# Optimization experiments

Measured on AMD Instinct MI355X. Metric: run time of the kernel, lower is better.

The kernel has to match this reference:

```python
import jax, jax.numpy as jnp
import numpy as np
from jax import lax

COUNT_NORM_FACTOR = 0.1


def setup_inputs() -> dict:
    key = jax.random.key(0)
    ks = jax.random.split(key, 8)
    B, NA, NT, D = 4096, 16, 16, 128
    task_embeds = jax.random.normal(ks[0], (B, NT, D), dtype=jnp.float32)
    task_nonag_counts = jax.random.uniform(ks[1], (B, NT), dtype=jnp.float32)
    agent_embeds = jax.random.normal(ks[2], (B, NA, D), dtype=jnp.float32)
    task_mask = jnp.zeros((B, NT), dtype=bool)
    agent_mask = jnp.zeros((B, NA), dtype=jnp.float32)  # 0 = active agent
    u = jax.random.uniform(ks[3], (NA, B, NT), dtype=jnp.float32,
                           minval=1e-6, maxval=1.0 - 1e-6)
    gumbels = -jnp.log(-jnp.log(u))
    W_count = jax.random.normal(ks[4], (2, D), dtype=jnp.float32) / np.sqrt(2.0)
    b_count = jnp.zeros((D,), dtype=jnp.float32)
    W_upd = jax.random.normal(ks[5], (2 * D, D), dtype=jnp.float32) / np.sqrt(2.0 * D)
    b_upd = jnp.zeros((D,), dtype=jnp.float32)
    return dict(task_embeds=task_embeds, task_nonag_counts=task_nonag_counts,
                agent_embeds=agent_embeds, task_mask=task_mask,
                agent_mask=agent_mask, gumbels=gumbels,
                W_count=W_count, b_count=b_count, W_upd=W_upd, b_upd=b_upd)


def _autoreg(task_embeds, task_nonag_counts, agent_embeds, task_mask,
             agent_mask, gumbels, W_count, b_count, W_upd, b_upd):
    B, NT, D = task_embeds.shape
    scale = jnp.sqrt(jnp.asarray(D, task_embeds.dtype))
    neg_min = jnp.finfo(task_embeds.dtype).min

    def step(carry, xs):
        te, counts = carry  # te: [B,NT,D], counts: [B,NT]
        ag_emb, g, amask = xs  # [B,D], [B,NT], [B]
        # count embedding: Linear(2, D) on stack([nonag, ag], -1)
        cnt_in = jnp.stack([task_nonag_counts, counts], axis=-1)  # [B,NT,2]
        cnt_e = cnt_in @ W_count + b_count  # [B,NT,D]
        # pointer logits
        logits = jnp.einsum('bd,btd->bt', ag_emb, te + cnt_e) / scale
        masked = jnp.where(task_mask, neg_min, logits)
        # RelaxedOneHotCategorical(temp=1).rsample via gumbel-softmax
        soft = jax.nn.softmax(masked + g, axis=-1)
        onehot = jax.nn.one_hot(jnp.argmax(soft, axis=-1), NT, dtype=soft.dtype)
        hard = onehot - lax.stop_gradient(soft) + soft
        agm = (1.0 - amask)[:, None]  # [B,1]
        hard = hard * agm
        hstop = lax.stop_gradient(hard)
        counts = counts + hstop * COUNT_NORM_FACTOR
        # embedding update: Linear(2D, D) on relu(concat([te, agent_embed]))
        upd_in = jnp.concatenate(
            [te, jnp.broadcast_to(ag_emb[:, None, :], (B, NT, D))], axis=-1)
        upd = jax.nn.relu(upd_in) @ W_upd + b_upd  # [B,NT,D]
        te = te + upd * hstop[..., None] * agm[..., None]
        return (te, counts), hard

    init = (task_embeds, jnp.zeros((B, NT), task_embeds.dtype))
    xs = (jnp.swapaxes(agent_embeds, 0, 1), gumbels, jnp.swapaxes(agent_mask, 0, 1))
    _, allocs = lax.scan(step, init, xs)  # [NA,B,NT]
    return jnp.swapaxes(allocs, 0, 1)  # [B,NA,NT]


def reference(task_embeds, task_nonag_counts, agent_embeds, task_mask,
              agent_mask, gumbels, W_count, b_count, W_upd, b_upd):
    return _autoreg(task_embeds, task_nonag_counts, agent_embeds, task_mask,
                    agent_mask, gumbels, W_count, b_count, W_upd, b_upd)
```

## Files before the change

kernel.cpp:

```cpp
#include <hip/hip_runtime.h>
#include <float.h>
#include <math.h>

#define NBATCH   4096
#define NAGENT   16
#define NTASK    16
#define DDIM     128
#define G        8
#define NTHREADS 512
#define SSEG     20

typedef float f32x2 __attribute__((ext_vector_type(2)));

template<int CTRL>
__device__ __forceinline__ float dppf(float x) {
    return __int_as_float(__builtin_amdgcn_update_dpp(
        0, __float_as_int(x), CTRL, 0xF, 0xF, true));
}
template<int CTRL>
__device__ __forceinline__ int dppi(int x) {
    return __builtin_amdgcn_update_dpp(0, x, CTRL, 0xF, 0xF, true);
}

template<int SEL>
__device__ __forceinline__ void pk_fma_b(f32x2& acc, f32x2 a, f32x2 b) {
    if constexpr (SEL == 0)
        asm("v_pk_fma_f32 %0, %1, %2, %0 op_sel:[0,0,0] op_sel_hi:[0,1,1]"
            : "+v"(acc) : "v"(a), "v"(b));
    else
        asm("v_pk_fma_f32 %0, %1, %2, %0 op_sel:[1,0,0] op_sel_hi:[1,1,1]"
            : "+v"(acc) : "v"(a), "v"(b));
}

__global__ __launch_bounds__(NTHREADS, 2)
void alloc_policy_kernel(const float* __restrict__ task_embeds,
                         const float* __restrict__ task_nonag,
                         const float* __restrict__ agent_embeds,
                         const unsigned char* __restrict__ task_mask,
                         const float* __restrict__ agent_mask,
                         const float* __restrict__ gumbels,
                         const float* __restrict__ W_count,
                         const float* __restrict__ b_count,
                         const float* __restrict__ W_upd,
                         const float* __restrict__ b_upd,
                         float* __restrict__ out)
{
    __shared__ __align__(16) float te[G][NTASK][DDIM];
    __shared__ __align__(16) float scr[G][16 * SSEG];
    __shared__ __align__(16) float4 sdots4[G][NAGENT];
    __shared__ __align__(16) float4 upd4[G];

    const int tid  = threadIdx.x;
    const int lane = tid & 63;
    const int w    = tid >> 6;
    const int b0   = blockIdx.x * G;
    const int gb_w = b0 + w;

    const bool h0 = (lane & 1) != 0;
    const bool h1 = (lane & 2) != 0;
    const bool h2 = (lane & 4) != 0;
    const bool h3 = (lane & 8) != 0;

    const int cg   = tid >> 4;
    const int iseg = tid & 15;
    const float bu = b_upd[cg * 4 + (tid & 3)];

    const float scalef = sqrtf(128.0f);

    f32x2 W01[16], W23[16];
    #pragma unroll
    for (int c = 0; c < 4; ++c)
        #pragma unroll
        for (int di = 0; di < 4; ++di) {
            const float4 wv = *(const float4*)(W_upd +
                (size_t)(iseg * 16 + c * 4 + di) * DDIM + cg * 4);
            W01[c * 4 + di] = f32x2{wv.x, wv.y};
            W23[c * 4 + di] = f32x2{wv.z, wv.w};
        }

    {
        const float4* src = (const float4*)(task_embeds + (size_t)b0 * NTASK * DDIM);
        float4* dst = (float4*)(&te[0][0][0]);
        #pragma unroll
        for (int k = 0; k < (G * NTASK * DDIM / 4) / NTHREADS; ++k)
            dst[k * NTHREADS + tid] = src[k * NTHREADS + tid];
    }

    {
        const int p = tid >> 2, q = tid & 3;
        const int g = p >> 4,  a = p & 15;
        const float* agp = agent_embeds + ((size_t)(b0 + g) * NAGENT + a) * DDIM + q * 32;
        float a0 = 0.f, a1 = 0.f, a2 = 0.f;
        #pragma unroll
        for (int c = 0; c < 8; ++c) {
            const float4 av = *(const float4*)(agp + c * 4);
            const float4 w0 = *(const float4*)(W_count + q * 32 + c * 4);
            const float4 w1 = *(const float4*)(W_count + DDIM + q * 32 + c * 4);
            const float4 bc = *(const float4*)(b_count + q * 32 + c * 4);
            a0 = fmaf(av.x, w0.x, a0); a0 = fmaf(av.y, w0.y, a0);
            a0 = fmaf(av.z, w0.z, a0); a0 = fmaf(av.w, w0.w, a0);
            a1 = fmaf(av.x, w1.x, a1); a1 = fmaf(av.y, w1.y, a1);
            a1 = fmaf(av.z, w1.z, a1); a1 = fmaf(av.w, w1.w, a1);
            a2 = fmaf(av.x, bc.x, a2); a2 = fmaf(av.y, bc.y, a2);
            a2 = fmaf(av.z, bc.z, a2); a2 = fmaf(av.w, bc.w, a2);
        }
        a0 += __shfl_xor(a0, 1); a0 += __shfl_xor(a0, 2);
        a1 += __shfl_xor(a1, 1); a1 += __shfl_xor(a1, 2);
        a2 += __shfl_xor(a2, 1); a2 += __shfl_xor(a2, 2);
        if (q == 0) sdots4[g][a] = make_float4(a0, a1, a2, 0.f);
    }

    const int tau = lane & 15;
    const float nn_my = task_nonag[gb_w * NTASK + tau];
    const unsigned char mask_my = task_mask[gb_w * NTASK + tau];
    float cc_my = 0.0f;

    const float* agbase = agent_embeds + (size_t)gb_w * NAGENT * DDIM;
    float2 ag2 = *(const float2*)(agbase + lane * 2);
    float  gum = gumbels[(size_t)gb_w * NTASK + tau];
    float  amk = agent_mask[(size_t)gb_w * NAGENT + 0];

    auto wave_dots = [&](float2 agv) -> float {
        float v[16];
        #pragma unroll
        for (int t = 0; t < 16; ++t) {
            const float2 t2 = *(const float2*)(&te[w][t][lane * 2]);
            v[t] = fmaf(agv.y, t2.y, agv.x * t2.x);
        }
        float p8[8];
        #pragma unroll
        for (int m2 = 0; m2 < 8; ++m2) {
            const float lo = v[2 * m2], hi = v[2 * m2 + 1];
            const float send = h0 ? lo : hi;
            const float mine = h0 ? hi : lo;
            p8[m2] = mine + dppf<0xB1>(send);
        }
        float p4[4];
        #pragma unroll
        for (int m2 = 0; m2 < 4; ++m2) {
            const float lo = p8[2 * m2], hi = p8[2 * m2 + 1];
            const float send = h1 ? lo : hi;
            const float mine = h1 ? hi : lo;
            p4[m2] = mine + dppf<0x4E>(send);
        }
        float p2v[2];
        #pragma unroll
        for (int m2 = 0; m2 < 2; ++m2) {
            const float lo = p4[2 * m2], hi = p4[2 * m2 + 1];
            const float send = h2 ? lo : hi;
            const float mine = h2 ? hi : lo;
            p2v[m2] = mine + __shfl_xor(send, 4);
        }
        float p1;
        {
            const float lo = p2v[0], hi = p2v[1];
            const float send = h3 ? lo : hi;
            const float mine = h3 ? hi : lo;
            p1 = mine + __shfl_xor(send, 8);
        }
        p1 += __shfl_xor(p1, 16);
        p1 += __shfl_xor(p1, 32);
        return p1;
    };

    __syncthreads();

    float p1_cur = wave_dots(ag2);

    for (int a = 0; a < NAGENT; ++a) {
        const float4 sd = sdots4[w][a];
        const float dot_total = p1_cur + fmaf(nn_my, sd.x, fmaf(cc_my, sd.y, sd.z));
        float z = dot_total / scalef;
        if (mask_my) z = -FLT_MAX;
        z = z + gum;

        float mz = z;
        mz = fmaxf(mz, dppf<0xB1>(mz));
        mz = fmaxf(mz, dppf<0x4E>(mz));
        mz = fmaxf(mz, __shfl_xor(mz, 4));
        mz = fmaxf(mz, __shfl_xor(mz, 8));
        const float e = expf(z - mz);
        float ss = e;
        ss += dppf<0xB1>(ss);
        ss += dppf<0x4E>(ss);
        ss += __shfl_xor(ss, 4);
        ss += __shfl_xor(ss, 8);
        const float sft = e / ss;

        float mx = sft;
        mx = fmaxf(mx, dppf<0xB1>(mx));
        mx = fmaxf(mx, dppf<0x4E>(mx));
        mx = fmaxf(mx, __shfl_xor(mx, 4));
        mx = fmaxf(mx, __shfl_xor(mx, 8));
        int cand = (sft == mx) ? tau : NTASK;
        cand = min(cand, dppi<0xB1>(cand));
        cand = min(cand, dppi<0x4E>(cand));
        cand = min(cand, __shfl_xor(cand, 4));
        cand = min(cand, __shfl_xor(cand, 8));
        const int bi = cand;

        const float agm = 1.0f - amk;
        const float onehot = (tau == bi) ? 1.0f : 0.0f;
        const float hh = ((onehot - sft) + sft) * agm;

        if (lane < 16)
            out[((size_t)gb_w * NAGENT + a) * NTASK + tau] = hh;
        cc_my = cc_my + hh * 0.1f;
        if (lane < 16 && tau == bi)
            upd4[w] = make_float4(__int_as_float(bi), hh, agm, 0.f);

        {
            const float2 tsel = *(const float2*)(&te[w][bi][lane * 2]);
            float2 r0, r1;
            r0.x = fmaxf(tsel.x, 0.f); r0.y = fmaxf(tsel.y, 0.f);
            r1.x = fmaxf(ag2.x, 0.f);  r1.y = fmaxf(ag2.y, 0.f);
            const int i0 = 2 * lane;
            const int i1 = 128 + 2 * lane;
            *(float2*)(&scr[w][(i0 >> 4) * SSEG + (i0 & 15)]) = r0;
            *(float2*)(&scr[w][(i1 >> 4) * SSEG + (i1 & 15)]) = r1;
        }

        const int an = (a + 1) & 15;
        const float2 ag2n = *(const float2*)(agbase + (size_t)an * DDIM + lane * 2);
        const float  gumn = gumbels[((size_t)an * NBATCH + gb_w) * NTASK + tau];
        const float  amkn = agent_mask[(size_t)gb_w * NAGENT + an];

        __syncthreads();

        f32x2 acc01[G], acc23[G];
        #pragma unroll
        for (int g = 0; g < G; ++g) { acc01[g] = f32x2{0.f, 0.f}; acc23[g] = f32x2{0.f, 0.f}; }
        #pragma unroll
        for (int c = 0; c < 4; ++c) {
            const int sb = iseg * SSEG + c * 4;
            #pragma unroll
            for (int g = 0; g < 8; ++g) {
                const float4 in4 = *(const float4*)(&scr[g][sb]);
                const f32x2 ixy = f32x2{in4.x, in4.y};
                const f32x2 izw = f32x2{in4.z, in4.w};
                pk_fma_b<0>(acc01[g], ixy, W01[c * 4 + 0]);
                pk_fma_b<1>(acc01[g], ixy, W01[c * 4 + 1]);
                pk_fma_b<0>(acc01[g], izw, W01[c * 4 + 2]);
                pk_fma_b<1>(acc01[g], izw, W01[c * 4 + 3]);
                pk_fma_b<0>(acc23[g], ixy, W23[c * 4 + 0]);
                pk_fma_b<1>(acc23[g], ixy, W23[c * 4 + 1]);
                pk_fma_b<0>(acc23[g], izw, W23[c * 4 + 2]);
                pk_fma_b<1>(acc23[g], izw, W23[c * 4 + 3]);
            }
        }
        float q16[16];
        #pragma unroll
        for (int m2 = 0; m2 < 16; ++m2) {
            const float lo = (m2 & 1) ? acc23[m2 >> 1].x : acc01[m2 >> 1].x;
            const float hi = (m2 & 1) ? acc23[m2 >> 1].y : acc01[m2 >> 1].y;
            const float send = h0 ? lo : hi;
            const float mine = h0 ? hi : lo;
            q16[m2] = mine + dppf<0xB1>(send);
        }
        float q8[8];
        #pragma unroll
        for (int m2 = 0; m2 < 8; ++m2) {
            const float lo = q16[2 * m2], hi = q16[2 * m2 + 1];
            const float send = h1 ? lo : hi;
            const float mine = h1 ? hi : lo;
            q8[m2] = mine + dppf<0x4E>(send);
        }
        float q4[4];
        #pragma unroll
        for (int m2 = 0; m2 < 4; ++m2) {
            const float lo = q8[2 * m2], hi = q8[2 * m2 + 1];
            const float send = h2 ? lo : hi;
            const float mine = h2 ? hi : lo;
            q4[m2] = mine + __shfl_xor(send, 4);
        }
        float q2[2];
        #pragma unroll
        for (int m2 = 0; m2 < 2; ++m2) {
            const float lo = q4[2 * m2], hi = q4[2 * m2 + 1];
            const float send = h3 ? lo : hi;
            const float mine = h3 ? hi : lo;
            q2[m2] = mine + __shfl_xor(send, 8);
        }

        float p1n = 0.f;
        if (a < NAGENT - 1) p1n = wave_dots(make_float2(ag2n.x, ag2n.y));

        #pragma unroll
        for (int hgi = 0; hgi < 2; ++hgi) {
            const int g = ((lane & 15) >> 2) + hgi * 4;
            const float4 u4 = upd4[g];
            const int ts = __float_as_int(u4.x);
            const float u = q2[hgi] + bu;
            const float addv = (u * u4.y) * u4.z;
            te[g][ts][cg * 4 + (tid & 3)] += addv;
        }
        __syncthreads();

        if (a < NAGENT - 1) {
            const float2 tn = *(const float2*)(&te[w][bi][lane * 2]);
            float pr = fmaf(ag2n.y, tn.y, ag2n.x * tn.x);
            pr += dppf<0xB1>(pr);
            pr += dppf<0x4E>(pr);
            pr += __shfl_xor(pr, 4);
            pr += __shfl_xor(pr, 8);
            pr += __shfl_xor(pr, 16);
            pr += __shfl_xor(pr, 32);
            p1_cur = (tau == bi) ? pr : p1n;
        }

        ag2 = ag2n; gum = gumn; amk = amkn;
    }
}

extern "C" void kernel_launch(void* const* d_in, const int* in_sizes, int n_in,
                              void* d_out, int out_size, void* d_ws, size_t ws_size,
                              hipStream_t stream) {
    const float*         task_embeds  = (const float*)d_in[0];
    const float*         task_nonag   = (const float*)d_in[1];
    const float*         agent_embeds = (const float*)d_in[2];
    const unsigned char* task_mask    = (const unsigned char*)d_in[3];
    const float*         agent_mask   = (const float*)d_in[4];
    const float*         gumbels      = (const float*)d_in[5];
    const float*         W_count      = (const float*)d_in[6];
    const float*         b_count      = (const float*)d_in[7];
    const float*         W_upd        = (const float*)d_in[8];
    const float*         b_upd        = (const float*)d_in[9];
    float* out = (float*)d_out;

    dim3 grid(NBATCH / G);
    dim3 block(NTHREADS);
    hipLaunchKernelGGL(alloc_policy_kernel, grid, block, 0, stream,
                       task_embeds, task_nonag, agent_embeds, task_mask,
                       agent_mask, gumbels, W_count, b_count, W_upd, b_upd, out);
}
```

Before: 131.2 us.

## Keep task embeddings in registers and stream W_upd from global per step

```diff
diff --git a/kernel.cpp b/kernel.cpp
--- a/kernel.cpp
+++ b/kernel.cpp
@@ -45,9 +45,9 @@
                          const float* __restrict__ b_upd,
                          float* __restrict__ out)
 {
-    __shared__ __align__(16) float te[G][NTASK][DDIM];
     __shared__ __align__(16) float scr[G][16 * SSEG];
     __shared__ __align__(16) float4 sdots4[G][NAGENT];
+    __shared__ __align__(16) float  uroute[G][DDIM];
     __shared__ __align__(16) float4 upd4[G];
 
     const int tid  = threadIdx.x;
@@ -66,24 +66,14 @@
     const float bu = b_upd[cg * 4 + (tid & 3)];
 
     const float scalef = sqrtf(128.0f);
-
-    f32x2 W01[16], W23[16];
-    #pragma unroll
-    for (int c = 0; c < 4; ++c)
-        #pragma unroll
-        for (int di = 0; di < 4; ++di) {
-            const float4 wv = *(const float4*)(W_upd +
-                (size_t)(iseg * 16 + c * 4 + di) * DDIM + cg * 4);
-            W01[c * 4 + di] = f32x2{wv.x, wv.y};
-            W23[c * 4 + di] = f32x2{wv.z, wv.w};
-        }
-
+    const float* wbase = W_upd + (size_t)(iseg * 16) * DDIM + cg * 4;
+
+    float2 te_reg[16];
     {
-        const float4* src = (const float4*)(task_embeds + (size_t)b0 * NTASK * DDIM);
-        float4* dst = (float4*)(&te[0][0][0]);
-        #pragma unroll
-        for (int k = 0; k < (G * NTASK * DDIM / 4) / NTHREADS; ++k)
-            dst[k * NTHREADS + tid] = src[k * NTHREADS + tid];
+        const float2* tb = (const float2*)(task_embeds + (size_t)gb_w * NTASK * DDIM);
+        #pragma unroll
+        for (int t = 0; t < 16; ++t)
+            te_reg[t] = tb[t * 64 + lane];
     }
 
     {
@@ -120,13 +110,13 @@
     float  gum = gumbels[(size_t)gb_w * NTASK + tau];
     float  amk = agent_mask[(size_t)gb_w * NAGENT + 0];
 
-    auto wave_dots = [&](float2 agv) -> float {
+    __syncthreads();
+
+    for (int a = 0; a < NAGENT; ++a) {
         float v[16];
         #pragma unroll
-        for (int t = 0; t < 16; ++t) {
-            const float2 t2 = *(const float2*)(&te[w][t][lane * 2]);
-            v[t] = fmaf(agv.y, t2.y, agv.x * t2.x);
-        }
+        for (int t = 0; t < 16; ++t)
+            v[t] = fmaf(ag2.y, te_reg[t].y, ag2.x * te_reg[t].x);
         float p8[8];
         #pragma unroll
         for (int m2 = 0; m2 < 8; ++m2) {
@@ -160,16 +150,9 @@
         }
         p1 += __shfl_xor(p1, 16);
         p1 += __shfl_xor(p1, 32);
-        return p1;
-    };
-
-    __syncthreads();
-
-    float p1_cur = wave_dots(ag2);
-
-    for (int a = 0; a < NAGENT; ++a) {
+
         const float4 sd = sdots4[w][a];
-        const float dot_total = p1_cur + fmaf(nn_my, sd.x, fmaf(cc_my, sd.y, sd.z));
+        const float dot_total = p1 + fmaf(nn_my, sd.x, fmaf(cc_my, sd.y, sd.z));
         float z = dot_total / scalef;
         if (mask_my) z = -FLT_MAX;
         z = z + gum;
@@ -198,6 +181,7 @@
         cand = min(cand, __shfl_xor(cand, 4));
         cand = min(cand, __shfl_xor(cand, 8));
         const int bi = cand;
+        const int bi_u = __builtin_amdgcn_readfirstlane(bi);
 
         const float agm = 1.0f - amk;
         const float onehot = (tau == bi) ? 1.0f : 0.0f;
@@ -210,7 +194,10 @@
             upd4[w] = make_float4(__int_as_float(bi), hh, agm, 0.f);
 
         {
-            const float2 tsel = *(const float2*)(&te[w][bi][lane * 2]);
+            float2 tsel = te_reg[0];
+            #pragma unroll
+            for (int t = 1; t < 16; ++t)
+                if (bi_u == t) tsel = te_reg[t];
             float2 r0, r1;
             r0.x = fmaxf(tsel.x, 0.f); r0.y = fmaxf(tsel.y, 0.f);
             r1.x = fmaxf(ag2.x, 0.f);  r1.y = fmaxf(ag2.y, 0.f);
@@ -225,6 +212,11 @@
         const float  gumn = gumbels[((size_t)an * NBATCH + gb_w) * NTASK + tau];
         const float  amkn = agent_mask[(size_t)gb_w * NAGENT + an];
 
+        float4 wA0 = *(const float4*)(wbase + 0 * DDIM);
+        float4 wA1 = *(const float4*)(wbase + 1 * DDIM);
+        float4 wA2 = *(const float4*)(wbase + 2 * DDIM);
+        float4 wA3 = *(const float4*)(wbase + 3 * DDIM);
+
         __syncthreads();
 
         f32x2 acc01[G], acc23[G];
@@ -232,21 +224,34 @@
         for (int g = 0; g < G; ++g) { acc01[g] = f32x2{0.f, 0.f}; acc23[g] = f32x2{0.f, 0.f}; }
         #pragma unroll
         for (int c = 0; c < 4; ++c) {
+            float4 wB0, wB1, wB2, wB3;
+            if (c < 3) {
+                const float* wn = wbase + (size_t)(c + 1) * 4 * DDIM;
+                wB0 = *(const float4*)(wn + 0 * DDIM);
+                wB1 = *(const float4*)(wn + 1 * DDIM);
+                wB2 = *(const float4*)(wn + 2 * DDIM);
+                wB3 = *(const float4*)(wn + 3 * DDIM);
+            }
             const int sb = iseg * SSEG + c * 4;
+            const f32x2 w01_0 = f32x2{wA0.x, wA0.y}, w23_0 = f32x2{wA0.z, wA0.w};
+            const f32x2 w01_1 = f32x2{wA1.x, wA1.y}, w23_1 = f32x2{wA1.z, wA1.w};
+            const f32x2 w01_2 = f32x2{wA2.x, wA2.y}, w23_2 = f32x2{wA2.z, wA2.w};
+            const f32x2 w01_3 = f32x2{wA3.x, wA3.y}, w23_3 = f32x2{wA3.z, wA3.w};
             #pragma unroll
             for (int g = 0; g < 8; ++g) {
                 const float4 in4 = *(const float4*)(&scr[g][sb]);
                 const f32x2 ixy = f32x2{in4.x, in4.y};
                 const f32x2 izw = f32x2{in4.z, in4.w};
-                pk_fma_b<0>(acc01[g], ixy, W01[c * 4 + 0]);
-                pk_fma_b<1>(acc01[g], ixy, W01[c * 4 + 1]);
-                pk_fma_b<0>(acc01[g], izw, W01[c * 4 + 2]);
-                pk_fma_b<1>(acc01[g], izw, W01[c * 4 + 3]);
-                pk_fma_b<0>(acc23[g], ixy, W23[c * 4 + 0]);
-                pk_fma_b<1>(acc23[g], ixy, W23[c * 4 + 1]);
-                pk_fma_b<0>(acc23[g], izw, W23[c * 4 + 2]);
-                pk_fma_b<1>(acc23[g], izw, W23[c * 4 + 3]);
+                pk_fma_b<0>(acc01[g], ixy, w01_0);
+                pk_fma_b<1>(acc01[g], ixy, w01_1);
+                pk_fma_b<0>(acc01[g], izw, w01_2);
+                pk_fma_b<1>(acc01[g], izw, w01_3);
+                pk_fma_b<0>(acc23[g], ixy, w23_0);
+                pk_fma_b<1>(acc23[g], ixy, w23_1);
+                pk_fma_b<0>(acc23[g], izw, w23_2);
+                pk_fma_b<1>(acc23[g], izw, w23_3);
             }
+            if (c < 3) { wA0 = wB0; wA1 = wB1; wA2 = wB2; wA3 = wB3; }
         }
         float q16[16];
         #pragma unroll
@@ -281,31 +286,20 @@
             const float mine = h3 ? hi : lo;
             q2[m2] = mine + __shfl_xor(send, 8);
         }
-
-        float p1n = 0.f;
-        if (a < NAGENT - 1) p1n = wave_dots(make_float2(ag2n.x, ag2n.y));
-
         #pragma unroll
         for (int hgi = 0; hgi < 2; ++hgi) {
             const int g = ((lane & 15) >> 2) + hgi * 4;
             const float4 u4 = upd4[g];
-            const int ts = __float_as_int(u4.x);
             const float u = q2[hgi] + bu;
-            const float addv = (u * u4.y) * u4.z;
-            te[g][ts][cg * 4 + (tid & 3)] += addv;
+            uroute[g][cg * 4 + (tid & 3)] = (u * u4.y) * u4.z;
         }
         __syncthreads();
 
-        if (a < NAGENT - 1) {
-            const float2 tn = *(const float2*)(&te[w][bi][lane * 2]);
-            float pr = fmaf(ag2n.y, tn.y, ag2n.x * tn.x);
-            pr += dppf<0xB1>(pr);
-            pr += dppf<0x4E>(pr);
-            pr += __shfl_xor(pr, 4);
-            pr += __shfl_xor(pr, 8);
-            pr += __shfl_xor(pr, 16);
-            pr += __shfl_xor(pr, 32);
-            p1_cur = (tau == bi) ? pr : p1n;
+        {
+            const float2 rt = *(const float2*)(&uroute[w][2 * lane]);
+            #pragma unroll
+            for (int t = 0; t < 16; ++t)
+                if (bi_u == t) { te_reg[t].x += rt.x; te_reg[t].y += rt.y; }
         }
 
         ag2 = ag2n; gum = gumn; amk = amkn;
```

Result: slower. 159.6 us (+21.7%).

## Halve block size, stream W_upd per step instead of holding it in registers

Applied to the files above, without the earlier changes.

```diff
diff --git a/kernel.cpp b/kernel.cpp
--- a/kernel.cpp
+++ b/kernel.cpp
@@ -6,8 +6,8 @@
 #define NAGENT   16
 #define NTASK    16
 #define DDIM     128
-#define G        8
-#define NTHREADS 512
+#define G        4
+#define NTHREADS 256
 #define SSEG     20
 
 typedef float f32x2 __attribute__((ext_vector_type(2)));
@@ -32,7 +32,20 @@
             : "+v"(acc) : "v"(a), "v"(b));
 }
 
-__global__ __launch_bounds__(NTHREADS, 2)
+__global__ void wperm_kernel(const float* __restrict__ W_upd,
+                             float4* __restrict__ wp) {
+    const int q    = blockIdx.x * 256 + threadIdx.x;
+    const int t    = q & 255;
+    const int rh   = q >> 8;
+    const int half = rh & 1;
+    const int row4 = rh >> 1;
+    const int i    = (t & 15) * 16 + row4;
+    const int col  = (t >> 4) * 8 + half * 4;
+    wp[q] = *(const float4*)(W_upd + (size_t)i * DDIM + col);
+}
+
+template<bool PERM>
+__global__ __launch_bounds__(NTHREADS, 4)
 void alloc_policy_kernel(const float* __restrict__ task_embeds,
                          const float* __restrict__ task_nonag,
                          const float* __restrict__ agent_embeds,
@@ -43,6 +56,7 @@
                          const float* __restrict__ b_count,
                          const float* __restrict__ W_upd,
                          const float* __restrict__ b_upd,
+                         const float4* __restrict__ wperm,
                          float* __restrict__ out)
 {
     __shared__ __align__(16) float te[G][NTASK][DDIM];
@@ -63,20 +77,9 @@
 
     const int cg   = tid >> 4;
     const int iseg = tid & 15;
-    const float bu = b_upd[cg * 4 + (tid & 3)];
+    const float bu = b_upd[cg * 8 + (lane & 7)];
 
     const float scalef = sqrtf(128.0f);
-
-    f32x2 W01[16], W23[16];
-    #pragma unroll
-    for (int c = 0; c < 4; ++c)
-        #pragma unroll
-        for (int di = 0; di < 4; ++di) {
-            const float4 wv = *(const float4*)(W_upd +
-                (size_t)(iseg * 16 + c * 4 + di) * DDIM + cg * 4);
-            W01[c * 4 + di] = f32x2{wv.x, wv.y};
-            W23[c * 4 + di] = f32x2{wv.z, wv.w};
-        }
 
     {
         const float4* src = (const float4*)(task_embeds + (size_t)b0 * NTASK * DDIM);
@@ -120,12 +123,14 @@
     float  gum = gumbels[(size_t)gb_w * NTASK + tau];
     float  amk = agent_mask[(size_t)gb_w * NAGENT + 0];
 
-    auto wave_dots = [&](float2 agv) -> float {
+    __syncthreads();
+
+    for (int a = 0; a < NAGENT; ++a) {
         float v[16];
         #pragma unroll
         for (int t = 0; t < 16; ++t) {
             const float2 t2 = *(const float2*)(&te[w][t][lane * 2]);
-            v[t] = fmaf(agv.y, t2.y, agv.x * t2.x);
+            v[t] = fmaf(ag2.y, t2.y, ag2.x * t2.x);
         }
         float p8[8];
         #pragma unroll
@@ -160,16 +165,9 @@
         }
         p1 += __shfl_xor(p1, 16);
         p1 += __shfl_xor(p1, 32);
-        return p1;
-    };
-
-    __syncthreads();
-
-    float p1_cur = wave_dots(ag2);
-
-    for (int a = 0; a < NAGENT; ++a) {
+
         const float4 sd = sdots4[w][a];
-        const float dot_total = p1_cur + fmaf(nn_my, sd.x, fmaf(cc_my, sd.y, sd.z));
+        const float dot_total = p1 + fmaf(nn_my, sd.x, fmaf(cc_my, sd.y, sd.z));
         float z = dot_total / scalef;
         if (mask_my) z = -FLT_MAX;
         z = z + gum;
@@ -227,32 +225,53 @@
 
         __syncthreads();
 
-        f32x2 acc01[G], acc23[G];
-        #pragma unroll
-        for (int g = 0; g < G; ++g) { acc01[g] = f32x2{0.f, 0.f}; acc23[g] = f32x2{0.f, 0.f}; }
+        f32x2 acc2[16];
+        #pragma unroll
+        for (int j = 0; j < 16; ++j) acc2[j] = f32x2{0.f, 0.f};
         #pragma unroll
         for (int c = 0; c < 4; ++c) {
-            const int sb = iseg * SSEG + c * 4;
+            float4 Wc[8];
+            if (PERM) {
+                const float4* wp = wperm + tid;
+                #pragma unroll
+                for (int rh = 0; rh < 8; ++rh)
+                    Wc[rh] = wp[(size_t)(c * 8 + rh) * 256];
+            } else {
+                #pragma unroll
+                for (int r = 0; r < 4; ++r) {
+                    const float* wrow = W_upd +
+                        (size_t)(iseg * 16 + c * 4 + r) * DDIM + cg * 8;
+                    Wc[r * 2]     = *(const float4*)(wrow);
+                    Wc[r * 2 + 1] = *(const float4*)(wrow + 4);
+                }
+            }
             #pragma unroll
-            for (int g = 0; g < 8; ++g) {
-                const float4 in4 = *(const float4*)(&scr[g][sb]);
+            for (int g = 0; g < G; ++g) {
+                const float4 in4 = *(const float4*)(&scr[g][iseg * SSEG + c * 4]);
                 const f32x2 ixy = f32x2{in4.x, in4.y};
                 const f32x2 izw = f32x2{in4.z, in4.w};
-                pk_fma_b<0>(acc01[g], ixy, W01[c * 4 + 0]);
-                pk_fma_b<1>(acc01[g], ixy, W01[c * 4 + 1]);
-                pk_fma_b<0>(acc01[g], izw, W01[c * 4 + 2]);
-                pk_fma_b<1>(acc01[g], izw, W01[c * 4 + 3]);
-                pk_fma_b<0>(acc23[g], ixy, W23[c * 4 + 0]);
-                pk_fma_b<1>(acc23[g], ixy, W23[c * 4 + 1]);
-                pk_fma_b<0>(acc23[g], izw, W23[c * 4 + 2]);
-                pk_fma_b<1>(acc23[g], izw, W23[c * 4 + 3]);
+                pk_fma_b<0>(acc2[g*4+0], ixy, f32x2{Wc[0].x, Wc[0].y});
+                pk_fma_b<0>(acc2[g*4+1], ixy, f32x2{Wc[0].z, Wc[0].w});
+                pk_fma_b<0>(acc2[g*4+2], ixy, f32x2{Wc[1].x, Wc[1].y});
+                pk_fma_b<0>(acc2[g*4+3], ixy, f32x2{Wc[1].z, Wc[1].w});
+                pk_fma_b<1>(acc2[g*4+0], ixy, f32x2{Wc[2].x, Wc[2].y});
+                pk_fma_b<1>(acc2[g*4+1], ixy, f32x2{Wc[2].z, Wc[2].w});
+                pk_fma_b<1>(acc2[g*4+2], ixy, f32x2{Wc[3].x, Wc[3].y});
+                pk_fma_b<1>(acc2[g*4+3], ixy, f32x2{Wc[3].z, Wc[3].w});
+                pk_fma_b<0>(acc2[g*4+0], izw, f32x2{Wc[4].x, Wc[4].y});
+                pk_fma_b<0>(acc2[g*4+1], izw, f32x2{Wc[4].z, Wc[4].w});
+                pk_fma_b<0>(acc2[g*4+2], izw, f32x2{Wc[5].x, Wc[5].y});
+                pk_fma_b<0>(acc2[g*4+3], izw, f32x2{Wc[5].z, Wc[5].w});
+                pk_fma_b<1>(acc2[g*4+0], izw, f32x2{Wc[6].x, Wc[6].y});
+                pk_fma_b<1>(acc2[g*4+1], izw, f32x2{Wc[6].z, Wc[6].w});
+                pk_fma_b<1>(acc2[g*4+2], izw, f32x2{Wc[7].x, Wc[7].y});
+                pk_fma_b<1>(acc2[g*4+3], izw, f32x2{Wc[7].z, Wc[7].w});
             }
         }
         float q16[16];
         #pragma unroll
         for (int m2 = 0; m2 < 16; ++m2) {
-            const float lo = (m2 & 1) ? acc23[m2 >> 1].x : acc01[m2 >> 1].x;
-            const float hi = (m2 & 1) ? acc23[m2 >> 1].y : acc01[m2 >> 1].y;
+            const float lo = acc2[m2].x, hi = acc2[m2].y;
             const float send = h0 ? lo : hi;
             const float mine = h0 ? hi : lo;
             q16[m2] = mine + dppf<0xB1>(send);
@@ -281,32 +300,16 @@
             const float mine = h3 ? hi : lo;
             q2[m2] = mine + __shfl_xor(send, 8);
         }
-
-        float p1n = 0.f;
-        if (a < NAGENT - 1) p1n = wave_dots(make_float2(ag2n.x, ag2n.y));
-
         #pragma unroll
         for (int hgi = 0; hgi < 2; ++hgi) {
-            const int g = ((lane & 15) >> 2) + hgi * 4;
+            const int g = 2 * hgi + ((lane >> 3) & 1);
             const float4 u4 = upd4[g];
             const int ts = __float_as_int(u4.x);
             const float u = q2[hgi] + bu;
             const float addv = (u * u4.y) * u4.z;
-            te[g][ts][cg * 4 + (tid & 3)] += addv;
+            te[g][ts][cg * 8 + (lane & 7)] += addv;
         }
         __syncthreads();
-
-        if (a < NAGENT - 1) {
-            const float2 tn = *(const float2*)(&te[w][bi][lane * 2]);
-            float pr = fmaf(ag2n.y, tn.y, ag2n.x * tn.x);
-            pr += dppf<0xB1>(pr);
-            pr += dppf<0x4E>(pr);
-            pr += __shfl_xor(pr, 4);
-            pr += __shfl_xor(pr, 8);
-            pr += __shfl_xor(pr, 16);
-            pr += __shfl_xor(pr, 32);
-            p1_cur = (tau == bi) ? pr : p1n;
-        }
 
         ag2 = ag2n; gum = gumn; amk = amkn;
     }
@@ -329,7 +332,18 @@
 
     dim3 grid(NBATCH / G);
     dim3 block(NTHREADS);
-    hipLaunchKernelGGL(alloc_policy_kernel, grid, block, 0, stream,
-                       task_embeds, task_nonag, agent_embeds, task_mask,
-                       agent_mask, gumbels, W_count, b_count, W_upd, b_upd, out);
-}
+
+    if (ws_size >= 2 * DDIM * DDIM * sizeof(float)) {
+        float4* wp = (float4*)d_ws;
+        hipLaunchKernelGGL(wperm_kernel, dim3(32), dim3(256), 0, stream, W_upd, wp);
+        hipLaunchKernelGGL(alloc_policy_kernel<true>, grid, block, 0, stream,
+                           task_embeds, task_nonag, agent_embeds, task_mask,
+                           agent_mask, gumbels, W_count, b_count, W_upd, b_upd,
+                           wp, out);
+    } else {
+        hipLaunchKernelGGL(alloc_policy_kernel<false>, grid, block, 0, stream,
+                           task_embeds, task_nonag, agent_embeds, task_mask,
+                           agent_mask, gumbels, W_count, b_count, W_upd, b_upd,
+                           (const float4*)nullptr, out);
+    }
+}
```

New measurement: 227.0 us. 73.1% more time.
